# Performance work log

Measured on AMD Instinct MI355X. Metric: run time of the kernel, lower is better.

Reference implementation:

```python
import jax, jax.numpy as jnp
import numpy as np

N_CLUSTERS = 128
NUM_ITERS = 10      # fixed Lloyd iterations
LN_EPS = 1e-5       # nn.LayerNorm default eps


def setup_inputs() -> dict:
    key = jax.random.key(0)
    k1, = jax.random.split(key, 1)
    B, N, D = 32, 8192, 64
    patches = jax.random.normal(k1, (B, N, D), dtype=jnp.float32)
    gamma = jnp.ones((D,), dtype=jnp.float32)   # LayerNorm weight
    beta = jnp.zeros((D,), dtype=jnp.float32)   # LayerNorm bias
    return {"patches": patches, "gamma": gamma, "beta": beta}


def _sq_dists(x, x2, c):
    # x: [B,N,D], x2: [B,N,1] (precomputed ||x||^2), c: [B,K,D] -> [B,N,K]
    c2 = jnp.sum(c * c, axis=-1)[:, None, :]                  # [B,1,K]
    return x2 + c2 - 2.0 * jnp.einsum('bnd,bkd->bnk', x, c)


def _kmeans(x):
    B, N, D = x.shape
    K = N_CLUSTERS
    centers0 = x[:, :K, :]                                    # deterministic init: first K points
    x2 = jnp.sum(x * x, axis=-1, keepdims=True)               # [B,N,1]

    def step(c, _):
        d = _sq_dists(x, x2, c)                               # [B,N,K]
        assign = jnp.argmin(d, axis=-1)                       # [B,N]
        oh = jax.nn.one_hot(assign, K, dtype=x.dtype)         # [B,N,K]
        counts = oh.sum(axis=1)                               # [B,K]
        sums = jnp.einsum('bnk,bnd->bkd', oh, x)              # [B,K,D]
        new_c = jnp.where(counts[..., None] > 0,
                          sums / jnp.maximum(counts, 1.0)[..., None],
                          c)                                  # keep empty clusters fixed
        return new_c, None

    centers, _ = jax.lax.scan(step, centers0, None, length=NUM_ITERS)
    dist = _sq_dists(x, x2, centers)                          # [B,N,K]
    soft = jax.nn.softmax(-dist, axis=-1)                     # soft assignment over clusters
    return centers, soft


def reference(patches, gamma, beta):
    # LayerNorm over last dim (biased variance, as in nn.LayerNorm)
    mu = jnp.mean(patches, axis=-1, keepdims=True)
    var = jnp.mean((patches - mu) ** 2, axis=-1, keepdims=True)
    xn = (patches - mu) * jax.lax.rsqrt(var + LN_EPS) * gamma + beta
    centers, soft = _kmeans(xn)
    return centers, soft
```

## Files before the change

### kernel.cpp

```cpp
#include <hip/hip_runtime.h>

#define BATCH 32
#define NPTS  8192
#define DIM   64
#define KC    128
#define NITER 10
#define LN_EPS 1e-5f


#define FMA4(acc, xv, cv) \
    acc = fmaf((xv).w, (cv).w, fmaf((xv).z, (cv).z, fmaf((xv).y, (cv).y, fmaf((xv).x, (cv).x, (acc)))))

#define DOT16(res, cbase) do {                                            \
    const float4* _c = (cbase);                                           \
    float _d0 = 0.f, _d1 = 0.f, _d2 = 0.f, _d3 = 0.f;                     \
    FMA4(_d0, x0, _c[0]);   FMA4(_d1, x1, _c[1]);                         \
    FMA4(_d2, x2, _c[2]);   FMA4(_d3, x3, _c[3]);                         \
    FMA4(_d0, x4, _c[4]);   FMA4(_d1, x5, _c[5]);                         \
    FMA4(_d2, x6, _c[6]);   FMA4(_d3, x7, _c[7]);                         \
    FMA4(_d0, x8, _c[8]);   FMA4(_d1, x9, _c[9]);                         \
    FMA4(_d2, x10, _c[10]); FMA4(_d3, x11, _c[11]);                       \
    FMA4(_d0, x12, _c[12]); FMA4(_d1, x13, _c[13]);                       \
    FMA4(_d2, x14, _c[14]); FMA4(_d3, x15, _c[15]);                       \
    res = (_d0 + _d1) + (_d2 + _d3);                                      \
} while (0)

#define SQ4(xv) do {                       \
    a0 = fmaf((xv).x, (xv).x, a0);         \
    a1 = fmaf((xv).y, (xv).y, a1);         \
    a2 = fmaf((xv).z, (xv).z, a2);         \
    a3 = fmaf((xv).w, (xv).w, a3);         \
} while (0)

#define LOAD_X16(ptr)                                              \
    const float4* xp = (const float4*)(ptr);                       \
    float4 x0 = xp[0], x1 = xp[1], x2 = xp[2], x3 = xp[3];         \
    float4 x4 = xp[4], x5 = xp[5], x6 = xp[6], x7 = xp[7];         \
    float4 x8 = xp[8], x9 = xp[9], x10 = xp[10], x11 = xp[11];     \
    float4 x12 = xp[12], x13 = xp[13], x14 = xp[14], x15 = xp[15]

__global__ __launch_bounds__(256) void ln_kernel(const float* __restrict__ patches,
                                                 const float* __restrict__ gamma,
                                                 const float* __restrict__ beta,
                                                 float* __restrict__ xn,
                                                 float* __restrict__ cen,
                                                 float* __restrict__ c2) {
    int row = blockIdx.x * 4 + (threadIdx.x >> 6);
    int lane = threadIdx.x & 63;
    size_t base = (size_t)row * DIM + lane;
    float x = patches[base];

    float s = x;
#pragma unroll
    for (int m = 32; m >= 1; m >>= 1) s += __shfl_xor(s, m, 64);
    float mu = s * (1.0f / 64.0f);
    float dx = x - mu;

    float v = dx * dx;
#pragma unroll
    for (int m = 32; m >= 1; m >>= 1) v += __shfl_xor(v, m, 64);
    float var = v * (1.0f / 64.0f);

    float val = dx * (1.0f / sqrtf(var + LN_EPS)) * gamma[lane] + beta[lane];
    xn[base] = val;

    int n = row & (NPTS - 1);
    int b = row >> 13;
    if (n < KC) {
        cen[((size_t)(b * KC + n)) * DIM + lane] = val;
        float q = val * val;
#pragma unroll
        for (int m = 32; m >= 1; m >>= 1) q += __shfl_xor(q, m, 64);
        if (lane == 0) c2[b * KC + n] = q;
    }
}

__global__ __launch_bounds__(512, 4) void assign_kernel(const float* __restrict__ xn,
                                                        const float* __restrict__ cen,
                                                        const float* __restrict__ c2,
                                                        float* __restrict__ part,
                                                        float* __restrict__ cntpart) {
    __shared__ float ls[KC * 65];
    __shared__ float lc[KC];
    for (int i = threadIdx.x; i < KC * 65; i += 512) ls[i] = 0.f;
    if (threadIdx.x < KC) lc[threadIdx.x] = 0.f;
    __syncthreads();

    int blk = blockIdx.x;
    int b = blk >> 4;
    int p = b * NPTS + ((blk & 15) << 9) + threadIdx.x;

    LOAD_X16(xn + (size_t)p * DIM);
    float a0 = 0.f, a1 = 0.f, a2 = 0.f, a3 = 0.f;
    SQ4(x0); SQ4(x1); SQ4(x2); SQ4(x3); SQ4(x4); SQ4(x5); SQ4(x6); SQ4(x7);
    SQ4(x8); SQ4(x9); SQ4(x10); SQ4(x11); SQ4(x12); SQ4(x13); SQ4(x14); SQ4(x15);
    float xsq = (a0 + a1) + (a2 + a3);

    const float4* cp = (const float4*)(cen + (size_t)b * KC * DIM);
    const float* c2p = c2 + b * KC;

    float best = 3.4e38f;
    int bi = 0;
    for (int k = 0; k < KC; ++k) {
        float dot;
        DOT16(dot, cp + k * 16);
        float t = xsq + c2p[k];
        float d = t - 2.0f * dot;
        if (d < best) { best = d; bi = k; }
    }

    float* dst = ls + bi * 65;
#define ATM4(j, xv)                            \
    atomicAdd(dst + 4 * (j) + 0, (xv).x);      \
    atomicAdd(dst + 4 * (j) + 1, (xv).y);      \
    atomicAdd(dst + 4 * (j) + 2, (xv).z);      \
    atomicAdd(dst + 4 * (j) + 3, (xv).w)
    ATM4(0, x0); ATM4(1, x1); ATM4(2, x2); ATM4(3, x3);
    ATM4(4, x4); ATM4(5, x5); ATM4(6, x6); ATM4(7, x7);
    ATM4(8, x8); ATM4(9, x9); ATM4(10, x10); ATM4(11, x11);
    ATM4(12, x12); ATM4(13, x13); ATM4(14, x14); ATM4(15, x15);
#undef ATM4
    atomicAdd(&lc[bi], 1.0f);
    __syncthreads();

    float* gp = part + (size_t)blk * KC * DIM;
    for (int i = threadIdx.x; i < KC * DIM; i += 512) {
        int k = i >> 6, d = i & 63;
        gp[i] = ls[k * 65 + d];
    }
    if (threadIdx.x < KC) cntpart[blk * KC + threadIdx.x] = lc[threadIdx.x];
}

__global__ __launch_bounds__(256) void update_kernel(const float* __restrict__ part,
                                                     const float* __restrict__ cntpart,
                                                     float* __restrict__ cen,
                                                     float* __restrict__ c2) {
    int row = blockIdx.x * 4 + (threadIdx.x >> 6);
    int lane = threadIdx.x & 63;
    int b = row >> 7;
    int k = row & (KC - 1);

    double s = 0.0;
    float cnt = 0.f;
#pragma unroll
    for (int sub = 0; sub < 16; ++sub) {
        s += (double)part[((size_t)(b * 16 + sub)) * KC * DIM + (size_t)k * DIM + lane];
        cnt += cntpart[(b * 16 + sub) * KC + k];
    }

    size_t idx = (size_t)row * DIM + lane;
    float old = cen[idx];
    float nc = (cnt > 0.f) ? ((float)s / cnt) : old;
    cen[idx] = nc;

    float q = nc * nc;
#pragma unroll
    for (int m = 32; m >= 1; m >>= 1) q += __shfl_xor(q, m, 64);
    if (lane == 0) c2[row] = q;
}

__global__ __launch_bounds__(512, 4) void final_kernel(const float* __restrict__ xn,
                                                       const float* __restrict__ cen,
                                                       const float* __restrict__ c2,
                                                       float* __restrict__ soft) {
    int b = blockIdx.x >> 4;
    int p = b * NPTS + ((blockIdx.x & 15) << 9) + threadIdx.x;

    LOAD_X16(xn + (size_t)p * DIM);
    float a0 = 0.f, a1 = 0.f, a2 = 0.f, a3 = 0.f;
    SQ4(x0); SQ4(x1); SQ4(x2); SQ4(x3); SQ4(x4); SQ4(x5); SQ4(x6); SQ4(x7);
    SQ4(x8); SQ4(x9); SQ4(x10); SQ4(x11); SQ4(x12); SQ4(x13); SQ4(x14); SQ4(x15);
    float xsq = (a0 + a1) + (a2 + a3);

    const float4* cp = (const float4*)(cen + (size_t)b * KC * DIM);
    const float* c2p = c2 + b * KC;

    float m = -3.4e38f;
    float ssum = 0.f;
    for (int k = 0; k < KC; ++k) {
        float dot;
        DOT16(dot, cp + k * 16);
        float t = xsq + c2p[k];
        float z = -(t - 2.0f * dot);
        if (z > m) {
            ssum = ssum * __expf(m - z) + 1.0f;
            m = z;
        } else {
            ssum += __expf(z - m);
        }
    }
    float rinv = 1.0f / ssum;

    float4* op = (float4*)(soft + (size_t)p * KC);
    for (int kb = 0; kb < KC / 4; ++kb) {
        float e[4];
#pragma unroll
        for (int u = 0; u < 4; ++u) {
            int k = kb * 4 + u;
            float dot;
            DOT16(dot, cp + k * 16);
            float t = xsq + c2p[k];
            float z = -(t - 2.0f * dot);
            e[u] = __expf(z - m) * rinv;
        }
        op[kb] = make_float4(e[0], e[1], e[2], e[3]);
    }
}

extern "C" void kernel_launch(void* const* d_in, const int* in_sizes, int n_in,
                              void* d_out, int out_size, void* d_ws, size_t ws_size,
                              hipStream_t stream) {
    (void)in_sizes; (void)n_in; (void)out_size; (void)ws_size;
    const float* patches = (const float*)d_in[0];
    const float* gamma = (const float*)d_in[1];
    const float* beta = (const float*)d_in[2];
    float* out = (float*)d_out;

    float* ws = (float*)d_ws;
    float* xn = ws;
    float* c2 = xn + (size_t)BATCH * NPTS * DIM;

    float* cen = out;
    float* soft = out + (size_t)BATCH * KC * DIM;
    float* part = soft;
    float* cntpart = part + (size_t)512 * KC * DIM;

    ln_kernel<<<BATCH * NPTS / 4, 256, 0, stream>>>(patches, gamma, beta, xn, cen, c2);

    for (int it = 0; it < NITER; ++it) {
        assign_kernel<<<BATCH * 16, 512, 0, stream>>>(xn, cen, c2, part, cntpart);
        update_kernel<<<BATCH * KC / 4, 256, 0, stream>>>(part, cntpart, cen, c2);
    }

    final_kernel<<<BATCH * 16, 512, 0, stream>>>(xn, cen, c2, soft);
}
```

Before: 2.192 ms.

## Stage point vectors in LDS instead of registers and halve block size

The assign and final kernels now keep each point's 64-float vector in shared memory, using a strided layout, instead of in 64 registers. This cuts register pressure. Blocks shrink from 512 to 256 points, so there are twice as many partial-sum blocks per batch, and update_kernel reduces across 32 partials instead of 16. The 64KB LDS per block limits occupancy, and every dot product now reads x from LDS, which adds LDS bandwidth pressure. The scatter phase reloads x from global memory.

```diff
diff --git a/kernel.cpp b/kernel.cpp
--- a/kernel.cpp
+++ b/kernel.cpp
@@ -7,37 +7,24 @@
 #define NITER 10
 #define LN_EPS 1e-5f
 
-
-#define FMA4(acc, xv, cv) \
-    acc = fmaf((xv).w, (cv).w, fmaf((xv).z, (cv).z, fmaf((xv).y, (cv).y, fmaf((xv).x, (cv).x, (acc)))))
-
-#define DOT16(res, cbase) do {                                            \
-    const float4* _c = (cbase);                                           \
-    float _d0 = 0.f, _d1 = 0.f, _d2 = 0.f, _d3 = 0.f;                     \
-    FMA4(_d0, x0, _c[0]);   FMA4(_d1, x1, _c[1]);                         \
-    FMA4(_d2, x2, _c[2]);   FMA4(_d3, x3, _c[3]);                         \
-    FMA4(_d0, x4, _c[4]);   FMA4(_d1, x5, _c[5]);                         \
-    FMA4(_d2, x6, _c[6]);   FMA4(_d3, x7, _c[7]);                         \
-    FMA4(_d0, x8, _c[8]);   FMA4(_d1, x9, _c[9]);                         \
-    FMA4(_d2, x10, _c[10]); FMA4(_d3, x11, _c[11]);                       \
-    FMA4(_d0, x12, _c[12]); FMA4(_d1, x13, _c[13]);                       \
-    FMA4(_d2, x14, _c[14]); FMA4(_d3, x15, _c[15]);                       \
-    res = (_d0 + _d1) + (_d2 + _d3);                                      \
+#define PTS_PER_BLK 256
+#define BLKS_PER_B  32
+#define NBLK        (BATCH * BLKS_PER_B)
+
+
+#define DOTL(res, cc) do {                                                 \
+    float _d0 = 0.f, _d1 = 0.f, _d2 = 0.f, _d3 = 0.f;                      \
+    _Pragma("unroll")                                                      \
+    for (int _j = 0; _j < 16; ++_j) {                                      \
+        float4 _xv = xs4[_j * PTS_PER_BLK + tid];                          \
+        float4 _cv = (cc)[_j];                                             \
+        float& _a = (_j & 3) == 0 ? _d0 : (_j & 3) == 1 ? _d1              \
+                    : (_j & 3) == 2 ? _d2 : _d3;                           \
+        _a = fmaf(_xv.w, _cv.w, fmaf(_xv.z, _cv.z,                         \
+             fmaf(_xv.y, _cv.y, fmaf(_xv.x, _cv.x, _a))));                 \
+    }                                                                      \
+    res = (_d0 + _d1) + (_d2 + _d3);                                       \
 } while (0)
-
-#define SQ4(xv) do {                       \
-    a0 = fmaf((xv).x, (xv).x, a0);         \
-    a1 = fmaf((xv).y, (xv).y, a1);         \
-    a2 = fmaf((xv).z, (xv).z, a2);         \
-    a3 = fmaf((xv).w, (xv).w, a3);         \
-} while (0)
-
-#define LOAD_X16(ptr)                                              \
-    const float4* xp = (const float4*)(ptr);                       \
-    float4 x0 = xp[0], x1 = xp[1], x2 = xp[2], x3 = xp[3];         \
-    float4 x4 = xp[4], x5 = xp[5], x6 = xp[6], x7 = xp[7];         \
-    float4 x8 = xp[8], x9 = xp[9], x10 = xp[10], x11 = xp[11];     \
-    float4 x12 = xp[12], x13 = xp[13], x14 = xp[14], x15 = xp[15]
 
 __global__ __launch_bounds__(256) void ln_kernel(const float* __restrict__ patches,
                                                  const float* __restrict__ gamma,
@@ -75,26 +62,35 @@
     }
 }
 
-__global__ __launch_bounds__(512, 4) void assign_kernel(const float* __restrict__ xn,
-                                                        const float* __restrict__ cen,
-                                                        const float* __restrict__ c2,
-                                                        float* __restrict__ part,
-                                                        float* __restrict__ cntpart) {
-    __shared__ float ls[KC * 65];
-    __shared__ float lc[KC];
-    for (int i = threadIdx.x; i < KC * 65; i += 512) ls[i] = 0.f;
-    if (threadIdx.x < KC) lc[threadIdx.x] = 0.f;
-    __syncthreads();
-
+__global__ __launch_bounds__(PTS_PER_BLK) void assign_kernel(const float* __restrict__ xn,
+                                                             const float* __restrict__ cen,
+                                                             const float* __restrict__ c2,
+                                                             float* __restrict__ part,
+                                                             float* __restrict__ cntpart) {
+    __shared__ __align__(16) char smem[65536];
+    float4* xs4 = (float4*)smem;
+    float* accf = (float*)smem;
+    float* cntf = (float*)(smem + 33280);
+
+    int tid = threadIdx.x;
     int blk = blockIdx.x;
-    int b = blk >> 4;
-    int p = b * NPTS + ((blk & 15) << 9) + threadIdx.x;
-
-    LOAD_X16(xn + (size_t)p * DIM);
+    int b = blk >> 5;
+    int pbase = b * NPTS + ((blk & 31) << 8);
+    int p = pbase + tid;
+
+    const float4* xp = (const float4*)(xn + (size_t)p * DIM);
     float a0 = 0.f, a1 = 0.f, a2 = 0.f, a3 = 0.f;
-    SQ4(x0); SQ4(x1); SQ4(x2); SQ4(x3); SQ4(x4); SQ4(x5); SQ4(x6); SQ4(x7);
-    SQ4(x8); SQ4(x9); SQ4(x10); SQ4(x11); SQ4(x12); SQ4(x13); SQ4(x14); SQ4(x15);
+#pragma unroll
+    for (int j = 0; j < 16; ++j) {
+        float4 t = xp[j];
+        xs4[j * PTS_PER_BLK + tid] = t;
+        a0 = fmaf(t.x, t.x, a0);
+        a1 = fmaf(t.y, t.y, a1);
+        a2 = fmaf(t.z, t.z, a2);
+        a3 = fmaf(t.w, t.w, a3);
+    }
     float xsq = (a0 + a1) + (a2 + a3);
+    __syncthreads();
 
     const float4* cp = (const float4*)(cen + (size_t)b * KC * DIM);
     const float* c2p = c2 + b * KC;
@@ -103,32 +99,37 @@
     int bi = 0;
     for (int k = 0; k < KC; ++k) {
         float dot;
-        DOT16(dot, cp + k * 16);
+        DOTL(dot, cp + k * 16);
         float t = xsq + c2p[k];
         float d = t - 2.0f * dot;
         if (d < best) { best = d; bi = k; }
     }
-
-    float* dst = ls + bi * 65;
-#define ATM4(j, xv)                            \
-    atomicAdd(dst + 4 * (j) + 0, (xv).x);      \
-    atomicAdd(dst + 4 * (j) + 1, (xv).y);      \
-    atomicAdd(dst + 4 * (j) + 2, (xv).z);      \
-    atomicAdd(dst + 4 * (j) + 3, (xv).w)
-    ATM4(0, x0); ATM4(1, x1); ATM4(2, x2); ATM4(3, x3);
-    ATM4(4, x4); ATM4(5, x5); ATM4(6, x6); ATM4(7, x7);
-    ATM4(8, x8); ATM4(9, x9); ATM4(10, x10); ATM4(11, x11);
-    ATM4(12, x12); ATM4(13, x13); ATM4(14, x14); ATM4(15, x15);
-#undef ATM4
-    atomicAdd(&lc[bi], 1.0f);
-    __syncthreads();
-
-    float* gp = part + (size_t)blk * KC * DIM;
-    for (int i = threadIdx.x; i < KC * DIM; i += 512) {
+    __syncthreads();
+
+    for (int i = tid; i < KC * 65; i += PTS_PER_BLK) accf[i] = 0.f;
+    if (tid < KC) cntf[tid] = 0.f;
+    __syncthreads();
+
+    {
+        float* dst = accf + bi * 65;
+#pragma unroll
+        for (int j = 0; j < 16; ++j) {
+            float4 t = xp[j];
+            atomicAdd(dst + 4 * j + 0, t.x);
+            atomicAdd(dst + 4 * j + 1, t.y);
+            atomicAdd(dst + 4 * j + 2, t.z);
+            atomicAdd(dst + 4 * j + 3, t.w);
+        }
+        atomicAdd(&cntf[bi], 1.0f);
+    }
+    __syncthreads();
+
+    float* gp = part + (size_t)blk * (KC * DIM);
+    for (int i = tid; i < KC * DIM; i += PTS_PER_BLK) {
         int k = i >> 6, d = i & 63;
-        gp[i] = ls[k * 65 + d];
-    }
-    if (threadIdx.x < KC) cntpart[blk * KC + threadIdx.x] = lc[threadIdx.x];
+        gp[i] = accf[k * 65 + d];
+    }
+    if (tid < KC) cntpart[blk * KC + tid] = cntf[tid];
 }
 
 __global__ __launch_bounds__(256) void update_kernel(const float* __restrict__ part,
@@ -143,9 +144,9 @@
     double s = 0.0;
     float cnt = 0.f;
 #pragma unroll
-    for (int sub = 0; sub < 16; ++sub) {
-        s += (double)part[((size_t)(b * 16 + sub)) * KC * DIM + (size_t)k * DIM + lane];
-        cnt += cntpart[(b * 16 + sub) * KC + k];
+    for (int sub = 0; sub < BLKS_PER_B; ++sub) {
+        s += (double)part[((size_t)(b * BLKS_PER_B + sub)) * (KC * DIM) + (size_t)k * DIM + lane];
+        cnt += cntpart[(b * BLKS_PER_B + sub) * KC + k];
     }
 
     size_t idx = (size_t)row * DIM + lane;
@@ -159,18 +160,32 @@
     if (lane == 0) c2[row] = q;
 }
 
-__global__ __launch_bounds__(512, 4) void final_kernel(const float* __restrict__ xn,
-                                                       const float* __restrict__ cen,
-                                                       const float* __restrict__ c2,
-                                                       float* __restrict__ soft) {
-    int b = blockIdx.x >> 4;
-    int p = b * NPTS + ((blockIdx.x & 15) << 9) + threadIdx.x;
-
-    LOAD_X16(xn + (size_t)p * DIM);
+__global__ __launch_bounds__(PTS_PER_BLK) void final_kernel(const float* __restrict__ xn,
+                                                            const float* __restrict__ cen,
+                                                            const float* __restrict__ c2,
+                                                            float* __restrict__ soft) {
+    __shared__ __align__(16) char smem[65536];
+    float4* xs4 = (float4*)smem;
+
+    int tid = threadIdx.x;
+    int blk = blockIdx.x;
+    int b = blk >> 5;
+    int pbase = b * NPTS + ((blk & 31) << 8);
+    int p = pbase + tid;
+
+    const float4* xp = (const float4*)(xn + (size_t)p * DIM);
     float a0 = 0.f, a1 = 0.f, a2 = 0.f, a3 = 0.f;
-    SQ4(x0); SQ4(x1); SQ4(x2); SQ4(x3); SQ4(x4); SQ4(x5); SQ4(x6); SQ4(x7);
-    SQ4(x8); SQ4(x9); SQ4(x10); SQ4(x11); SQ4(x12); SQ4(x13); SQ4(x14); SQ4(x15);
+#pragma unroll
+    for (int j = 0; j < 16; ++j) {
+        float4 t = xp[j];
+        xs4[j * PTS_PER_BLK + tid] = t;
+        a0 = fmaf(t.x, t.x, a0);
+        a1 = fmaf(t.y, t.y, a1);
+        a2 = fmaf(t.z, t.z, a2);
+        a3 = fmaf(t.w, t.w, a3);
+    }
     float xsq = (a0 + a1) + (a2 + a3);
+    __syncthreads();
 
     const float4* cp = (const float4*)(cen + (size_t)b * KC * DIM);
     const float* c2p = c2 + b * KC;
@@ -179,7 +194,7 @@
     float ssum = 0.f;
     for (int k = 0; k < KC; ++k) {
         float dot;
-        DOT16(dot, cp + k * 16);
+        DOTL(dot, cp + k * 16);
         float t = xsq + c2p[k];
         float z = -(t - 2.0f * dot);
         if (z > m) {
@@ -198,7 +213,7 @@
         for (int u = 0; u < 4; ++u) {
             int k = kb * 4 + u;
             float dot;
-            DOT16(dot, cp + k * 16);
+            DOTL(dot, cp + k * 16);
             float t = xsq + c2p[k];
             float z = -(t - 2.0f * dot);
             e[u] = __expf(z - m) * rinv;
@@ -223,14 +238,14 @@
     float* cen = out;
     float* soft = out + (size_t)BATCH * KC * DIM;
     float* part = soft;
-    float* cntpart = part + (size_t)512 * KC * DIM;
+    float* cntpart = part + (size_t)NBLK * KC * DIM;
 
     ln_kernel<<<BATCH * NPTS / 4, 256, 0, stream>>>(patches, gamma, beta, xn, cen, c2);
 
     for (int it = 0; it < NITER; ++it) {
-        assign_kernel<<<BATCH * 16, 512, 0, stream>>>(xn, cen, c2, part, cntpart);
+        assign_kernel<<<NBLK, PTS_PER_BLK, 0, stream>>>(xn, cen, c2, part, cntpart);
         update_kernel<<<BATCH * KC / 4, 256, 0, stream>>>(part, cntpart, cen, c2);
     }
 
-    final_kernel<<<BATCH * 16, 512, 0, stream>>>(xn, cen, c2, soft);
-}
+    final_kernel<<<NBLK, PTS_PER_BLK, 0, stream>>>(xn, cen, c2, soft);
+}
```

Result: slower. 2.706 ms (+23.5%).
